# Optimization experiments

Hardware: AMD Instinct MI355X
Metric: run time of the kernel (lower is better)

## Reference

```python
import jax, jax.numpy as jnp
import numpy as np

EPS = 1.0 / 137.0
NUM_HEADS = 16


def yat_dense(x, kernel, bias, alpha):
    y = jnp.einsum('btc,cf->btf', x, kernel)
    x2 = jnp.sum(x * x, axis=-1, keepdims=True)          # [B,T,1]
    k2 = jnp.sum(kernel * kernel, axis=0)                 # [F]
    y = (y * y) / (x2 + k2 - 2.0 * y + EPS)
    out_f = kernel.shape[1]
    scale = (jnp.sqrt(jnp.float32(out_f)) / jnp.log1p(jnp.float32(out_f))) ** alpha
    return y * scale + bias


def setup_inputs() -> dict:
    key = jax.random.key(0)
    ks = jax.random.split(key, 6)
    B, T, C = 2, 1024, 1024
    x = jax.random.normal(ks[0], (B, T, C), dtype=jnp.float32)
    mask = jnp.tril(jnp.ones((T, T), dtype=bool))[None, None, :, :]  # causal [1,1,T,T]
    w_qkv = jax.random.normal(ks[1], (C, 3 * C), dtype=jnp.float32) * 0.02
    b_qkv = jnp.zeros((3 * C,), dtype=jnp.float32)
    alpha_qkv = jnp.ones((1,), dtype=jnp.float32)
    w_proj = jax.random.normal(ks[2], (C, C), dtype=jnp.float32) * 0.02
    b_proj = jnp.zeros((C,), dtype=jnp.float32)
    alpha_proj = jnp.ones((1,), dtype=jnp.float32)
    alpha_attn = jnp.ones((1,), dtype=jnp.float32)
    return {"x": x, "mask": mask, "w_qkv": w_qkv, "b_qkv": b_qkv,
            "alpha_qkv": alpha_qkv, "w_proj": w_proj, "b_proj": b_proj,
            "alpha_proj": alpha_proj, "alpha_attn": alpha_attn}


def reference(x, mask, w_qkv, b_qkv, alpha_qkv, w_proj, b_proj, alpha_proj, alpha_attn):
    B, T, C = x.shape
    head_dim = C // NUM_HEADS
    scale = jnp.log1p(jnp.float32(head_dim))
    inv_scale = (head_dim / scale) ** alpha_attn  # [1]

    qkv = yat_dense(x, w_qkv, b_qkv, alpha_qkv)               # [B,T,3C]
    qkv = qkv.reshape(B, T, 3, NUM_HEADS, head_dim)
    q, k, v = jnp.moveaxis(qkv, 2, 0)                         # each [B,T,H,hd]
    # NOTE: source transposes with (0,3,1,2) -> [B, head_dim, T, H]; reproduced faithfully.
    q = jnp.transpose(q, (0, 3, 1, 2))
    k = jnp.transpose(k, (0, 3, 1, 2))
    v = jnp.transpose(v, (0, 3, 1, 2))

    dot = jnp.einsum('bhid,bhjd->bhij', q, k)                 # [B,hd,T,T]
    sq_dot = dot * dot
    q2 = jnp.sum(q * q, axis=-1, keepdims=True)               # [B,hd,T,1]
    k2 = jnp.sum(k * k, axis=-1, keepdims=True).transpose(0, 1, 3, 2)  # [B,hd,1,T]
    sq_dist = q2 + k2 - 2.0 * dot
    attn = sq_dot / (sq_dist + EPS)
    attn = attn * inv_scale
    attn = jnp.where(mask, attn, jnp.finfo(jnp.float32).min)
    attn = jax.nn.softmax(attn, axis=-1)

    out = jnp.einsum('bhij,bhjd->bhid', attn, v)              # [B,hd,T,H]
    out = out.transpose(0, 2, 1, 3).reshape(B, T, C)
    out = yat_dense(out, w_proj, b_proj, alpha_proj)
    return out
```

## Files before the change

kernel.cpp:

```cpp
#include <hip/hip_runtime.h>
#include <math.h>

#define YAT_EPS (1.0f / 137.0f)


typedef __bf16 bf16x8 __attribute__((ext_vector_type(8)));
typedef float floatx4 __attribute__((ext_vector_type(4)));
typedef unsigned int uintx4 __attribute__((ext_vector_type(4)));

__device__ __forceinline__ float fast_rcp(float x) {
#if __has_builtin(__builtin_amdgcn_rcpf)
    return __builtin_amdgcn_rcpf(x);
#else
    return 1.0f / x;
#endif
}
__device__ __forceinline__ float fast_exp2(float x) {
#if __has_builtin(__builtin_amdgcn_exp2f)
    return __builtin_amdgcn_exp2f(x);
#else
    return exp2f(x);
#endif
}

__device__ __forceinline__ unsigned short f32_bf16(float f) {
    unsigned u = __builtin_bit_cast(unsigned, f);
    u += 0x7fffu + ((u >> 16) & 1u);
    return (unsigned short)(u >> 16);
}
__device__ __forceinline__ float bf16_f32(unsigned short h) {
    unsigned u = ((unsigned)h) << 16;
    return __builtin_bit_cast(float, u);
}

__global__ void convtrans_kernel(
    const float* __restrict__ W, unsigned short* __restrict__ th,
    unsigned short* __restrict__ tl, float* __restrict__ k2, int K, int N)
{
    __shared__ float t[32][33];
    int tx = threadIdx.x, ty = threadIdx.y;
    int n0 = blockIdx.x * 32, k0 = blockIdx.y * 32;
    #pragma unroll
    for (int r = 0; r < 4; ++r)
        t[ty + r * 8][tx] = W[(size_t)(k0 + ty + r * 8) * N + n0 + tx];
    __syncthreads();
    #pragma unroll
    for (int r = 0; r < 4; ++r) {
        int nl = ty + r * 8;
        float v = t[tx][nl];
        unsigned short h = f32_bf16(v);
        th[(size_t)(n0 + nl) * K + k0 + tx] = h;
        tl[(size_t)(n0 + nl) * K + k0 + tx] = f32_bf16(v - bf16_f32(h));
        float s = v * v;
        #pragma unroll
        for (int m = 16; m > 0; m >>= 1) s += __shfl_xor(s, m, 32);
        if (tx == 0) atomicAdd(&k2[n0 + nl], s);
    }
}

__global__ __launch_bounds__(256) void convx_kernel(
    const float* __restrict__ x, unsigned short* __restrict__ hi,
    unsigned short* __restrict__ lo, float* __restrict__ x2x)
{
    __shared__ float red[4];
    const int row = blockIdx.x, tid = threadIdx.x;
    float4 v = *(const float4*)(x + (size_t)row * 1024 + tid * 4);
    float vv[4] = {v.x, v.y, v.z, v.w};
    unsigned short hh[4], ll[4];
    float s = 0.0f;
    #pragma unroll
    for (int e = 0; e < 4; ++e) {
        hh[e] = f32_bf16(vv[e]);
        ll[e] = f32_bf16(vv[e] - bf16_f32(hh[e]));
        s = fmaf(vv[e], vv[e], s);
    }
    *(ushort4*)(hi + (size_t)row * 1024 + tid * 4) =
        make_ushort4(hh[0], hh[1], hh[2], hh[3]);
    *(ushort4*)(lo + (size_t)row * 1024 + tid * 4) =
        make_ushort4(ll[0], ll[1], ll[2], ll[3]);
    #pragma unroll
    for (int off = 32; off > 0; off >>= 1) s += __shfl_down(s, off, 64);
    if ((tid & 63) == 0) red[tid >> 6] = s;
    __syncthreads();
    if (tid == 0) x2x[row] = red[0] + red[1] + red[2] + red[3];
}

template <int BM, int MODE>
__global__ __launch_bounds__(256) void gemm_yat_mfma_kernel(
    const unsigned short* __restrict__ Ah, const unsigned short* __restrict__ Al,
    const unsigned short* __restrict__ Bh, const unsigned short* __restrict__ Bl,
    const float* __restrict__ bias, const float* __restrict__ x2,
    const float* __restrict__ k2, const float* __restrict__ alphap,
    float* __restrict__ out, int N, int K, float scale_base)
{
    constexpr int TM = BM / 32;
    constexpr int NI = (BM * 128 + 16384) / 4096;
    __shared__ __align__(16) unsigned short sbuf[BM * 64 + 8192];

    const int tid = threadIdx.x;
    const int w = tid >> 6, l = tid & 63;
    const int lane16 = l & 15, quad = l >> 4;
    const int wm = w & 1, wn = w >> 1;
    const int m0 = blockIdx.y * BM, n0 = blockIdx.x * 128;

    floatx4 acc[TM][4];
    #pragma unroll
    for (int tm = 0; tm < TM; ++tm)
        #pragma unroll
        for (int tn = 0; tn < 4; ++tn)
            acc[tm][tn] = (floatx4){0.f, 0.f, 0.f, 0.f};

    for (int k0 = 0; k0 < K; k0 += 32) {
        __syncthreads();
        #pragma unroll
        for (int i = 0; i < NI; ++i) {
            const int o = (i * 4 + w) * 1024;
            const unsigned short* gp;
            if (o < BM * 128) {
                const unsigned short* g = (o < BM * 64) ? Ah : Al;
                const int oo = (o < BM * 64) ? o : o - BM * 64;
                gp = g + (size_t)(m0 + (oo >> 6) + (l >> 2)) * K + k0 + (l & 3) * 8;
            } else {
                const int ob = o - BM * 128;
                const unsigned short* g = (ob < 8192) ? Bh : Bl;
                const int oo = ob & 8191;
                gp = g + (size_t)(n0 + (oo >> 6) + (l >> 2)) * K + k0 + (l & 3) * 8;
            }
            __builtin_amdgcn_global_load_lds(
                (const __attribute__((address_space(1))) unsigned int*)gp,
                (__attribute__((address_space(3))) unsigned int*)((char*)sbuf + o),
                16, 0, 0);
        }
        __syncthreads();

        bf16x8 afh[TM], afl[TM], bfh[4], bfl[4];
        #pragma unroll
        for (int tm = 0; tm < TM; ++tm) {
            const int base = (wm * (BM / 2) + tm * 16 + lane16) * 32 + quad * 8;
            afh[tm] = *(const bf16x8*)(sbuf + base);
            afl[tm] = *(const bf16x8*)(sbuf + BM * 32 + base);
        }
        #pragma unroll
        for (int tn = 0; tn < 4; ++tn) {
            const int nb = (wn * 64 + tn * 16 + lane16) * 32 + quad * 8;
            bfh[tn] = *(const bf16x8*)(sbuf + BM * 64 + nb);
            bfl[tn] = *(const bf16x8*)(sbuf + BM * 64 + 4096 + nb);
        }
        #pragma unroll
        for (int tm = 0; tm < TM; ++tm)
            #pragma unroll
            for (int tn = 0; tn < 4; ++tn) {
                acc[tm][tn] = __builtin_amdgcn_mfma_f32_16x16x32_bf16(
                    afh[tm], bfh[tn], acc[tm][tn], 0, 0, 0);
                acc[tm][tn] = __builtin_amdgcn_mfma_f32_16x16x32_bf16(
                    afh[tm], bfl[tn], acc[tm][tn], 0, 0, 0);
                acc[tm][tn] = __builtin_amdgcn_mfma_f32_16x16x32_bf16(
                    afl[tm], bfh[tn], acc[tm][tn], 0, 0, 0);
            }
    }

    const float scale = powf(scale_base, alphap[0]);
    #pragma unroll
    for (int tm = 0; tm < TM; ++tm) {
        #pragma unroll
        for (int tn = 0; tn < 4; ++tn) {
            const int n = n0 + wn * 64 + tn * 16 + lane16;
            const float kk = k2[n];
            const float bb = bias[n];
            const int mrow = m0 + wm * (BM / 2) + tm * 16 + quad * 4;
            float4 r4;
            float* rp = (float*)&r4;
            #pragma unroll
            for (int r = 0; r < 4; ++r) {
                const float y = acc[tm][tn][r];
                const float den = x2[mrow + r] + kk - 2.0f * y + YAT_EPS;
                rp[r] = y * y / den * scale + bb;
            }
            if (MODE == 0) {
                #pragma unroll
                for (int r = 0; r < 4; ++r)
                    out[(size_t)(mrow + r) * N + n] = rp[r];
            } else {
                const int s = n >> 10, hh = (n >> 6) & 15, dd = n & 63;
                const int bb2 = m0 >> 10;
                const int t0 = (mrow & 1023);
                *(float4*)&out[((size_t)((bb2 * 3 + s) * 64 + dd) * 16 + hh)
                               * 1024 + t0] = r4;
            }
        }
    }
}

__global__ __launch_bounds__(256) void prep_q_kernel(
    const float* __restrict__ qkvT, unsigned short* __restrict__ QP,
    float* __restrict__ q2k)
{
    const int idx = blockIdx.x * 256 + threadIdx.x;
    const int b = idx >> 16, dt = idx & 65535;
    const int d = dt >> 10, t = dt & 1023;
    const float* src = qkvT + ((size_t)(b * 3 * 64) + d) * 16384 + t;
    float q[16]; float s2 = 0.f;
    unsigned short hi[16], lo[16];
    #pragma unroll
    for (int h = 0; h < 16; ++h) {
        q[h] = src[h * 1024];
        s2 = fmaf(q[h], q[h], s2);
        hi[h] = f32_bf16(q[h]);
        lo[h] = f32_bf16(q[h] - bf16_f32(hi[h]));
    }
    q2k[idx] = s2;
    unsigned short* dst = QP + (size_t)idx * 32;
    #pragma unroll
    for (int h4 = 0; h4 < 4; ++h4) {
        *(ushort4*)(dst + h4 * 4) =
            make_ushort4(hi[h4*4], hi[h4*4+1], hi[h4*4+2], hi[h4*4+3]);
        *(ushort4*)(dst + 16 + h4 * 4) =
            make_ushort4(lo[h4*4], lo[h4*4+1], lo[h4*4+2], lo[h4*4+3]);
    }
}

__global__ __launch_bounds__(256) void prep_k_kernel(
    const float* __restrict__ qkvT, unsigned short* __restrict__ KP,
    float* __restrict__ k2k)
{
    const int idx = blockIdx.x * 256 + threadIdx.x;
    const int b = idx >> 16, dt = idx & 65535;
    const int d = dt >> 10, t = dt & 1023;
    const float* src = qkvT + ((size_t)((b * 3 + 1) * 64) + d) * 16384 + t;
    float k[16]; float s2 = 0.f;
    unsigned short hi[16], lo[16];
    #pragma unroll
    for (int h = 0; h < 16; ++h) {
        k[h] = src[h * 1024];
        s2 = fmaf(k[h], k[h], s2);
        hi[h] = f32_bf16(k[h]);
        lo[h] = f32_bf16(k[h] - bf16_f32(hi[h]));
    }
    k2k[idx] = s2;
    unsigned short* dst = KP + (size_t)b * 6291456 + (size_t)dt * 32;
    #pragma unroll
    for (int h4 = 0; h4 < 4; ++h4) {
        *(ushort4*)(dst + h4 * 4) =
            make_ushort4(hi[h4*4], hi[h4*4+1], hi[h4*4+2], hi[h4*4+3]);
        *(ushort4*)(dst + 16 + h4 * 4) =
            make_ushort4(lo[h4*4], lo[h4*4+1], lo[h4*4+2], lo[h4*4+3]);
    }
}

__global__ __launch_bounds__(256) void prep_v_kernel(
    const float* __restrict__ qkvT, unsigned short* __restrict__ VP)
{
    const int idx = blockIdx.x * 256 + threadIdx.x;
    const int h = idx & 15;
    const int quad = (idx >> 4) & 3;
    const int jt2 = (idx >> 6) & 31;
    const int d = (idx >> 11) & 63;
    const int b = idx >> 17;
    const float* src = qkvT + ((size_t)((b * 3 + 2) * 64) + d) * 16384
                            + h * 1024 + jt2 * 32 + quad * 4;
    float4 v0 = *(const float4*)(src);
    float4 v1 = *(const float4*)(src + 16);
    float vv[8] = {v0.x, v0.y, v0.z, v0.w, v1.x, v1.y, v1.z, v1.w};
    unsigned short hi[8], lo[8];
    #pragma unroll
    for (int e = 0; e < 8; ++e) {
        hi[e] = f32_bf16(vv[e]);
        lo[e] = f32_bf16(vv[e] - bf16_f32(hi[e]));
    }
    unsigned short* dst = VP + (size_t)b * 6291456 + 2097152
                             + d * 32768 + jt2 * 1024 + quad * 128 + h * 8;
    *(ushort4*)(dst)       = make_ushort4(hi[0], hi[1], hi[2], hi[3]);
    *(ushort4*)(dst + 4)   = make_ushort4(hi[4], hi[5], hi[6], hi[7]);
    *(ushort4*)(dst + 512) = make_ushort4(lo[0], lo[1], lo[2], lo[3]);
    *(ushort4*)(dst + 516) = make_ushort4(lo[4], lo[5], lo[6], lo[7]);
}

__global__ __launch_bounds__(256) void yat_attn_mfma2_kernel(
    const unsigned short* __restrict__ QP,
    const unsigned short* __restrict__ KVU,
    const float* __restrict__ k2k, const float* __restrict__ q2k,
    const float* __restrict__ alphap,
    unsigned short* __restrict__ attn_h, unsigned short* __restrict__ attn_l,
    float* __restrict__ x2a)
{
    const int tid = threadIdx.x;
    const int lane = tid & 63, w = tid >> 6;
    const int lane16 = lane & 15, quad = lane >> 4;
    const int d = blockIdx.x, c = blockIdx.y, b = blockIdx.z;

    const float isc =
        powf(64.0f / log1pf(64.0f), alphap[0]) * 1.44269504f;

    const unsigned short* kp = KVU + (size_t)b * 6291456 + d * 32768;
    const unsigned short* vp = KVU + (size_t)b * 6291456 + 2097152 + d * 32768;
    const unsigned short* qp = QP + (size_t)(b * 65536 + d * 1024) * 32;
    const float* k2bd = k2k + b * 65536 + d * 1024;
    const float* q2bd = q2k + b * 65536 + d * 1024;

    const int ti0 = c * 4 + w;
    const int tiA = ti0, tiB = 63 - ti0;

    const bf16x8 qA = *(const bf16x8*)(qp + (tiA * 16 + lane16) * 32 + quad * 8);
    const bf16x8 qB = *(const bf16x8*)(qp + (tiB * 16 + lane16) * 32 + quad * 8);
    const float q2A = q2bd[tiA * 16 + lane16] + YAT_EPS;
    const float q2B = q2bd[tiB * 16 + lane16] + YAT_EPS;
    const int iA = tiA * 16 + lane16;
    const int iB = tiB * 16 + lane16;

    floatx4 OA = (floatx4){0.f, 0.f, 0.f, 0.f};
    floatx4 OB = (floatx4){0.f, 0.f, 0.f, 0.f};
    float lsA = 0.f, lsB = 0.f;

    const int lastA = tiA >> 1, lastB = tiB >> 1;

    for (int jt2 = 0; jt2 <= lastB; ++jt2) {
        const int j0 = jt2 * 32;
        const unsigned short* kp0 = kp + (j0 + lane16) * 32;
        const unsigned short* kp1 = kp + (j0 + 16 + lane16) * 32;
        const bf16x8 k0a = *(const bf16x8*)(kp0 + quad * 8);
        const bf16x8 k0b = *(const bf16x8*)(kp0 + ((quad ^ 2) * 8));
        const bf16x8 k1a = *(const bf16x8*)(kp1 + quad * 8);
        const bf16x8 k1b = *(const bf16x8*)(kp1 + ((quad ^ 2) * 8));
        const unsigned short* vpj = vp + jt2 * 1024 + quad * 128 + lane16 * 8;
        const bf16x8 vh = *(const bf16x8*)(vpj);
        const bf16x8 vl = *(const bf16x8*)(vpj + 512);
        const float4 k20 = *(const float4*)(k2bd + j0 + quad * 4);
        const float4 k21 = *(const float4*)(k2bd + j0 + 16 + quad * 4);
        const float k2r[8] = {k20.x, k20.y, k20.z, k20.w,
                              k21.x, k21.y, k21.z, k21.w};
        const int jbase0 = j0 + quad * 4;

        #pragma unroll
        for (int half = 0; half < 2; ++half) {
            if (half == 0 && jt2 > lastA) continue;
            const bf16x8 qf = half ? qB : qA;
            const float q2e = half ? q2B : q2A;
            const int iM = half ? iB : iA;
            floatx4 S0 = __builtin_amdgcn_mfma_f32_16x16x32_bf16(
                k0a, qf, (floatx4){0.f, 0.f, 0.f, 0.f}, 0, 0, 0);
            S0 = __builtin_amdgcn_mfma_f32_16x16x32_bf16(k0b, qf, S0, 0, 0, 0);
            floatx4 S1 = __builtin_amdgcn_mfma_f32_16x16x32_bf16(
                k1a, qf, (floatx4){0.f, 0.f, 0.f, 0.f}, 0, 0, 0);
            S1 = __builtin_amdgcn_mfma_f32_16x16x32_bf16(k1b, qf, S1, 0, 0, 0);

            float p[8], lsum = 0.f;
            #pragma unroll
            for (int e = 0; e < 8; ++e) {
                const float s = (e < 4) ? S0[e & 3] : S1[e & 3];
                const int j = jbase0 + (e >> 2) * 16 + (e & 3);
                const float den = fmaf(-2.f, s, q2e + k2r[e]);
                float pe = fast_exp2(s * s * fast_rcp(den) * isc);
                pe = (j <= iM) ? pe : 0.f;
                lsum += pe;
                p[e] = pe;
            }
            if (half) lsB += lsum; else lsA += lsum;

            unsigned ph32[4], pl32[4];
            #pragma unroll
            for (int e2 = 0; e2 < 4; ++e2) {
                const unsigned b0 = __builtin_bit_cast(unsigned, p[e2 * 2]);
                const unsigned b1 = __builtin_bit_cast(unsigned, p[e2 * 2 + 1]);
                const unsigned r0 = b0 + 0x7fffu + ((b0 >> 16) & 1u);
                const unsigned r1 = b1 + 0x7fffu + ((b1 >> 16) & 1u);
                ph32[e2] = (r0 >> 16) | (r1 & 0xFFFF0000u);
                const float f0 = p[e2 * 2] -
                    __builtin_bit_cast(float, r0 & 0xFFFF0000u);
                const float f1 = p[e2 * 2 + 1] -
                    __builtin_bit_cast(float, r1 & 0xFFFF0000u);
                pl32[e2] = (__builtin_bit_cast(unsigned, f0) >> 16) |
                           (__builtin_bit_cast(unsigned, f1) & 0xFFFF0000u);
            }
            const bf16x8 Ph = __builtin_bit_cast(bf16x8,
                (uintx4){ph32[0], ph32[1], ph32[2], ph32[3]});
            const bf16x8 Pl = __builtin_bit_cast(bf16x8,
                (uintx4){pl32[0], pl32[1], pl32[2], pl32[3]});

            floatx4 O = half ? OB : OA;
            O = __builtin_amdgcn_mfma_f32_16x16x32_bf16(Ph, vh, O, 0, 0, 0);
            O = __builtin_amdgcn_mfma_f32_16x16x32_bf16(Pl, vh, O, 0, 0, 0);
            O = __builtin_amdgcn_mfma_f32_16x16x32_bf16(Ph, vl, O, 0, 0, 0);
            if (half) OB = O; else OA = O;
        }
    }

    #pragma unroll
    for (int half = 0; half < 2; ++half) {
        float ls = half ? lsB : lsA;
        const floatx4 O = half ? OB : OA;
        const int ti = half ? tiB : tiA;
        ls += __shfl_xor(ls, 16, 64);
        ls += __shfl_xor(ls, 32, 64);
        const float linv = 1.0f / ls;
        #pragma unroll
        for (int r = 0; r < 4; ++r) {
            const float lr = __shfl(linv, quad * 4 + r, 16);
            const float v = O[r] * lr;
            const int i = ti * 16 + quad * 4 + r;
            const size_t off =
                ((size_t)(b * 1024 + i)) * 1024 + d * 16 + lane16;
            const unsigned short vh16 = f32_bf16(v);
            attn_h[off] = vh16;
            attn_l[off] = f32_bf16(v - bf16_f32(vh16));
            float s2 = v * v;
            s2 += __shfl_xor(s2, 1, 64);
            s2 += __shfl_xor(s2, 2, 64);
            s2 += __shfl_xor(s2, 4, 64);
            s2 += __shfl_xor(s2, 8, 64);
            if (lane16 == 0) atomicAdd(&x2a[b * 1024 + i], s2);
        }
    }
}

extern "C" void kernel_launch(void* const* d_in, const int* in_sizes, int n_in,
                              void* d_out, int out_size, void* d_ws, size_t ws_size,
                              hipStream_t stream)
{
    const float* x          = (const float*)d_in[0];
    const float* w_qkv      = (const float*)d_in[2];
    const float* b_qkv      = (const float*)d_in[3];
    const float* alpha_qkv  = (const float*)d_in[4];
    const float* w_proj     = (const float*)d_in[5];
    const float* b_proj     = (const float*)d_in[6];
    const float* alpha_proj = (const float*)d_in[7];
    const float* alpha_attn = (const float*)d_in[8];
    float* out = (float*)d_out;

    float* ws = (float*)d_ws;
    float*          qkvT = ws;
    unsigned short* WtQh = (unsigned short*)(ws + 6291456);
    unsigned short* WtQl = (unsigned short*)(ws + 7864320);
    unsigned short* WtPh = (unsigned short*)(ws + 9437184);
    unsigned short* WtPl = (unsigned short*)(ws + 9961472);
    unsigned short* xh   = (unsigned short*)(ws + 10485760);
    unsigned short* xl   = (unsigned short*)(ws + 11534336);
    float* x2x  = ws + 12582912;
    float* x2a  = ws + 12584960;
    float* k2q  = ws + 12587008;
    float* k2p  = ws + 12590080;
    float* k2k  = ws + 12591104;
    float* q2k  = ws + 12722176;
    unsigned short* attn_h = WtQh;
    unsigned short* attn_l = WtQl;
    unsigned short* QP = xh;
    unsigned short* KVU = (unsigned short*)qkvT;

    hipMemsetAsync(x2a, 0, (2048 + 3072 + 1024) * sizeof(float), stream);

    convtrans_kernel<<<dim3(96, 32), dim3(32, 8), 0, stream>>>(
        w_qkv, WtQh, WtQl, k2q, 1024, 3072);
    convtrans_kernel<<<dim3(32, 32), dim3(32, 8), 0, stream>>>(
        w_proj, WtPh, WtPl, k2p, 1024, 1024);
    convx_kernel<<<2048, 256, 0, stream>>>(x, xh, xl, x2x);

    const float sb_qkv = sqrtf(3072.0f) / log1pf(3072.0f);
    gemm_yat_mfma_kernel<64, 1><<<dim3(24, 32), 256, 0, stream>>>(
        xh, xl, WtQh, WtQl, b_qkv, x2x, k2q, alpha_qkv, qkvT,
        3072, 1024, sb_qkv);

    prep_q_kernel<<<512, 256, 0, stream>>>(qkvT, QP, q2k);
    prep_k_kernel<<<512, 256, 0, stream>>>(qkvT, KVU, k2k);
    prep_v_kernel<<<1024, 256, 0, stream>>>(qkvT, KVU);

    yat_attn_mfma2_kernel<<<dim3(64, 8, 2), 256, 0, stream>>>(
        QP, KVU, k2k, q2k, alpha_attn, attn_h, attn_l, x2a);

    const float sb_proj = sqrtf(1024.0f) / log1pf(1024.0f);
    gemm_yat_mfma_kernel<64, 0><<<dim3(8, 32), 256, 0, stream>>>(
        attn_h, attn_l, WtPh, WtPl, b_proj, x2a, k2p, alpha_proj, out,
        1024, 1024, sb_proj);
}
```

Baseline: 268.4 us.

## Fuse Q/K/V bf16 packing into QKV GEMM epilogue via permuted weight columns

Permutes the columns of the transposed QKV weight so each 128-wide GEMM tile holds all 16 heads for 8 head dims. The GEMM epilogue stages results through LDS and writes the split-bf16 Q/K/V layouts and squared norms directly. This removes the fp32 qkvT intermediate and the three prep kernels, along with their global memory round trip. The cost is an epilogue with extra syncs, scattered 2-byte stores for V, and Q now sharing the KVU buffer region.

```diff
diff --git a/kernel.cpp b/kernel.cpp
--- a/kernel.cpp
+++ b/kernel.cpp
@@ -33,6 +33,7 @@
     return __builtin_bit_cast(float, u);
 }
 
+template <bool PERM>
 __global__ void convtrans_kernel(
     const float* __restrict__ W, unsigned short* __restrict__ th,
     unsigned short* __restrict__ tl, float* __restrict__ k2, int K, int N)
@@ -47,14 +48,20 @@
     #pragma unroll
     for (int r = 0; r < 4; ++r) {
         int nl = ty + r * 8;
+        int nn = n0 + nl;
+        int nw = nn;
+        if (PERM) {
+            nw = (nn & ~1023) | (((nn & 63) >> 3) << 7)
+               | (((nn >> 6) & 15) << 3) | (nn & 7);
+        }
         float v = t[tx][nl];
         unsigned short h = f32_bf16(v);
-        th[(size_t)(n0 + nl) * K + k0 + tx] = h;
-        tl[(size_t)(n0 + nl) * K + k0 + tx] = f32_bf16(v - bf16_f32(h));
+        th[(size_t)nw * K + k0 + tx] = h;
+        tl[(size_t)nw * K + k0 + tx] = f32_bf16(v - bf16_f32(h));
         float s = v * v;
         #pragma unroll
         for (int m = 16; m > 0; m >>= 1) s += __shfl_xor(s, m, 32);
-        if (tx == 0) atomicAdd(&k2[n0 + nl], s);
+        if (tx == 0) atomicAdd(&k2[nn], s);
     }
 }
 
@@ -91,7 +98,9 @@
     const unsigned short* __restrict__ Bh, const unsigned short* __restrict__ Bl,
     const float* __restrict__ bias, const float* __restrict__ x2,
     const float* __restrict__ k2, const float* __restrict__ alphap,
-    float* __restrict__ out, int N, int K, float scale_base)
+    float* __restrict__ out, int N, int K, float scale_base,
+    unsigned short* __restrict__ kvu, float* __restrict__ q2k,
+    float* __restrict__ k2k)
 {
     constexpr int TM = BM / 32;
     constexpr int NI = (BM * 128 + 16384) / 4096;
@@ -160,123 +169,110 @@
     }
 
     const float scale = powf(scale_base, alphap[0]);
-    #pragma unroll
-    for (int tm = 0; tm < TM; ++tm) {
-        #pragma unroll
-        for (int tn = 0; tn < 4; ++tn) {
-            const int n = n0 + wn * 64 + tn * 16 + lane16;
-            const float kk = k2[n];
-            const float bb = bias[n];
-            const int mrow = m0 + wm * (BM / 2) + tm * 16 + quad * 4;
-            float4 r4;
-            float* rp = (float*)&r4;
+
+    if (MODE == 0) {
+        #pragma unroll
+        for (int tm = 0; tm < TM; ++tm) {
             #pragma unroll
-            for (int r = 0; r < 4; ++r) {
-                const float y = acc[tm][tn][r];
-                const float den = x2[mrow + r] + kk - 2.0f * y + YAT_EPS;
-                rp[r] = y * y / den * scale + bb;
-            }
-            if (MODE == 0) {
+            for (int tn = 0; tn < 4; ++tn) {
+                const int n = n0 + wn * 64 + tn * 16 + lane16;
+                const float kk = k2[n];
+                const float bb = bias[n];
+                const int mrow = m0 + wm * (BM / 2) + tm * 16 + quad * 4;
                 #pragma unroll
-                for (int r = 0; r < 4; ++r)
-                    out[(size_t)(mrow + r) * N + n] = rp[r];
+                for (int r = 0; r < 4; ++r) {
+                    const float y = acc[tm][tn][r];
+                    const float den = x2[mrow + r] + kk - 2.0f * y + YAT_EPS;
+                    out[(size_t)(mrow + r) * N + n] =
+                        y * y / den * scale + bb;
+                }
+            }
+        }
+    } else {
+        float* lds = (float*)sbuf;
+        const int s_ = n0 >> 10;
+        const int dblk = (n0 >> 7) & 7;
+        const int b_ = m0 >> 10;
+        const int tl = tid >> 3;
+        const int ddr = tid & 7;
+        const int d_glob = dblk * 8 + ddr;
+
+        #pragma unroll
+        for (int half = 0; half < 2; ++half) {
+            __syncthreads();
+            if (wm == half) {
+                #pragma unroll
+                for (int tm = 0; tm < TM; ++tm) {
+                    #pragma unroll
+                    for (int tn = 0; tn < 4; ++tn) {
+                        const int n = n0 + wn * 64 + tn * 16 + lane16;
+                        const int hcol = (n >> 3) & 15;
+                        const int norig = (n & ~1023) | (hcol << 6)
+                                        | (dblk << 3) | (n & 7);
+                        const float kk = k2[norig];
+                        const float bb = bias[norig];
+                        const int mrow = m0 + wm * 32 + tm * 16 + quad * 4;
+                        const int tbase = tm * 16 + quad * 4;
+                        const int col = wn * 64 + tn * 16 + lane16;
+                        #pragma unroll
+                        for (int r = 0; r < 4; ++r) {
+                            const float y = acc[tm][tn][r];
+                            const float den =
+                                x2[mrow + r] + kk - 2.0f * y + YAT_EPS;
+                            lds[(tbase + r) * 132 + col] =
+                                y * y / den * scale + bb;
+                        }
+                    }
+                }
+            }
+            __syncthreads();
+
+            float y[16];
+            #pragma unroll
+            for (int h = 0; h < 16; ++h)
+                y[h] = lds[tl * 132 + h * 8 + ddr];
+            const int t_glob = (m0 & 1023) + half * 32 + tl;
+
+            if (s_ < 2) {
+                unsigned short hb[16], lb[16];
+                float s2 = 0.f;
+                #pragma unroll
+                for (int h = 0; h < 16; ++h) {
+                    hb[h] = f32_bf16(y[h]);
+                    lb[h] = f32_bf16(y[h] - bf16_f32(hb[h]));
+                    s2 = fmaf(y[h], y[h], s2);
+                }
+                unsigned short* dst = kvu + (size_t)b_ * 6291456
+                    + (s_ == 0 ? 4194304u : 0u)
+                    + ((size_t)(d_glob * 1024 + t_glob)) * 32;
+                #pragma unroll
+                for (int h4 = 0; h4 < 4; ++h4) {
+                    *(ushort4*)(dst + h4 * 4) = make_ushort4(
+                        hb[h4*4], hb[h4*4+1], hb[h4*4+2], hb[h4*4+3]);
+                    *(ushort4*)(dst + 16 + h4 * 4) = make_ushort4(
+                        lb[h4*4], lb[h4*4+1], lb[h4*4+2], lb[h4*4+3]);
+                }
+                float* sq = (s_ == 0) ? q2k : k2k;
+                sq[b_ * 65536 + d_glob * 1024 + t_glob] = s2;
             } else {
-                const int s = n >> 10, hh = (n >> 6) & 15, dd = n & 63;
-                const int bb2 = m0 >> 10;
-                const int t0 = (mrow & 1023);
-                *(float4*)&out[((size_t)((bb2 * 3 + s) * 64 + dd) * 16 + hh)
-                               * 1024 + t0] = r4;
-            }
-        }
-    }
-}
-
-__global__ __launch_bounds__(256) void prep_q_kernel(
-    const float* __restrict__ qkvT, unsigned short* __restrict__ QP,
-    float* __restrict__ q2k)
-{
-    const int idx = blockIdx.x * 256 + threadIdx.x;
-    const int b = idx >> 16, dt = idx & 65535;
-    const int d = dt >> 10, t = dt & 1023;
-    const float* src = qkvT + ((size_t)(b * 3 * 64) + d) * 16384 + t;
-    float q[16]; float s2 = 0.f;
-    unsigned short hi[16], lo[16];
-    #pragma unroll
-    for (int h = 0; h < 16; ++h) {
-        q[h] = src[h * 1024];
-        s2 = fmaf(q[h], q[h], s2);
-        hi[h] = f32_bf16(q[h]);
-        lo[h] = f32_bf16(q[h] - bf16_f32(hi[h]));
-    }
-    q2k[idx] = s2;
-    unsigned short* dst = QP + (size_t)idx * 32;
-    #pragma unroll
-    for (int h4 = 0; h4 < 4; ++h4) {
-        *(ushort4*)(dst + h4 * 4) =
-            make_ushort4(hi[h4*4], hi[h4*4+1], hi[h4*4+2], hi[h4*4+3]);
-        *(ushort4*)(dst + 16 + h4 * 4) =
-            make_ushort4(lo[h4*4], lo[h4*4+1], lo[h4*4+2], lo[h4*4+3]);
-    }
-}
-
-__global__ __launch_bounds__(256) void prep_k_kernel(
-    const float* __restrict__ qkvT, unsigned short* __restrict__ KP,
-    float* __restrict__ k2k)
-{
-    const int idx = blockIdx.x * 256 + threadIdx.x;
-    const int b = idx >> 16, dt = idx & 65535;
-    const int d = dt >> 10, t = dt & 1023;
-    const float* src = qkvT + ((size_t)((b * 3 + 1) * 64) + d) * 16384 + t;
-    float k[16]; float s2 = 0.f;
-    unsigned short hi[16], lo[16];
-    #pragma unroll
-    for (int h = 0; h < 16; ++h) {
-        k[h] = src[h * 1024];
-        s2 = fmaf(k[h], k[h], s2);
-        hi[h] = f32_bf16(k[h]);
-        lo[h] = f32_bf16(k[h] - bf16_f32(hi[h]));
-    }
-    k2k[idx] = s2;
-    unsigned short* dst = KP + (size_t)b * 6291456 + (size_t)dt * 32;
-    #pragma unroll
-    for (int h4 = 0; h4 < 4; ++h4) {
-        *(ushort4*)(dst + h4 * 4) =
-            make_ushort4(hi[h4*4], hi[h4*4+1], hi[h4*4+2], hi[h4*4+3]);
-        *(ushort4*)(dst + 16 + h4 * 4) =
-            make_ushort4(lo[h4*4], lo[h4*4+1], lo[h4*4+2], lo[h4*4+3]);
-    }
-}
-
-__global__ __launch_bounds__(256) void prep_v_kernel(
-    const float* __restrict__ qkvT, unsigned short* __restrict__ VP)
-{
-    const int idx = blockIdx.x * 256 + threadIdx.x;
-    const int h = idx & 15;
-    const int quad = (idx >> 4) & 3;
-    const int jt2 = (idx >> 6) & 31;
-    const int d = (idx >> 11) & 63;
-    const int b = idx >> 17;
-    const float* src = qkvT + ((size_t)((b * 3 + 2) * 64) + d) * 16384
-                            + h * 1024 + jt2 * 32 + quad * 4;
-    float4 v0 = *(const float4*)(src);
-    float4 v1 = *(const float4*)(src + 16);
-    float vv[8] = {v0.x, v0.y, v0.z, v0.w, v1.x, v1.y, v1.z, v1.w};
-    unsigned short hi[8], lo[8];
-    #pragma unroll
-    for (int e = 0; e < 8; ++e) {
-        hi[e] = f32_bf16(vv[e]);
-        lo[e] = f32_bf16(vv[e] - bf16_f32(hi[e]));
-    }
-    unsigned short* dst = VP + (size_t)b * 6291456 + 2097152
-                             + d * 32768 + jt2 * 1024 + quad * 128 + h * 8;
-    *(ushort4*)(dst)       = make_ushort4(hi[0], hi[1], hi[2], hi[3]);
-    *(ushort4*)(dst + 4)   = make_ushort4(hi[4], hi[5], hi[6], hi[7]);
-    *(ushort4*)(dst + 512) = make_ushort4(lo[0], lo[1], lo[2], lo[3]);
-    *(ushort4*)(dst + 516) = make_ushort4(lo[4], lo[5], lo[6], lo[7]);
+                const int j = t_glob;
+                const int jt2 = j >> 5;
+                const int e = ((j >> 4) & 1) * 4 + (j & 3);
+                const int qd = (j >> 2) & 3;
+                unsigned short* dst = kvu + (size_t)b_ * 6291456 + 2097152
+                    + d_glob * 32768 + jt2 * 1024 + qd * 128 + e;
+                #pragma unroll
+                for (int h = 0; h < 16; ++h) {
+                    const unsigned short vh = f32_bf16(y[h]);
+                    dst[h * 8] = vh;
+                    dst[512 + h * 8] = f32_bf16(y[h] - bf16_f32(vh));
+                }
+            }
+        }
+    }
 }
 
 __global__ __launch_bounds__(256) void yat_attn_mfma2_kernel(
-    const unsigned short* __restrict__ QP,
     const unsigned short* __restrict__ KVU,
     const float* __restrict__ k2k, const float* __restrict__ q2k,
     const float* __restrict__ alphap,
@@ -293,7 +289,7 @@
 
     const unsigned short* kp = KVU + (size_t)b * 6291456 + d * 32768;
     const unsigned short* vp = KVU + (size_t)b * 6291456 + 2097152 + d * 32768;
-    const unsigned short* qp = QP + (size_t)(b * 65536 + d * 1024) * 32;
+    const unsigned short* qp = KVU + (size_t)b * 6291456 + 4194304 + d * 32768;
     const float* k2bd = k2k + b * 65536 + d * 1024;
     const float* q2bd = q2k + b * 65536 + d * 1024;
 
@@ -427,7 +423,7 @@
     float* out = (float*)d_out;
 
     float* ws = (float*)d_ws;
-    float*          qkvT = ws;
+    unsigned short* KVU  = (unsigned short*)ws;
     unsigned short* WtQh = (unsigned short*)(ws + 6291456);
     unsigned short* WtQl = (unsigned short*)(ws + 7864320);
     unsigned short* WtPh = (unsigned short*)(ws + 9437184);
@@ -442,31 +438,25 @@
     float* q2k  = ws + 12722176;
     unsigned short* attn_h = WtQh;
     unsigned short* attn_l = WtQl;
-    unsigned short* QP = xh;
-    unsigned short* KVU = (unsigned short*)qkvT;
 
     hipMemsetAsync(x2a, 0, (2048 + 3072 + 1024) * sizeof(float), stream);
 
-    convtrans_kernel<<<dim3(96, 32), dim3(32, 8), 0, stream>>>(
+    convtrans_kernel<true><<<dim3(96, 32), dim3(32, 8), 0, stream>>>(
         w_qkv, WtQh, WtQl, k2q, 1024, 3072);
-    convtrans_kernel<<<dim3(32, 32), dim3(32, 8), 0, stream>>>(
+    convtrans_kernel<false><<<dim3(32, 32), dim3(32, 8), 0, stream>>>(
         w_proj, WtPh, WtPl, k2p, 1024, 1024);
     convx_kernel<<<2048, 256, 0, stream>>>(x, xh, xl, x2x);
 
     const float sb_qkv = sqrtf(3072.0f) / log1pf(3072.0f);
-    gemm_yat_mfma_kernel<64, 1><<<dim3(24, 32), 256, 0, stream>>>(
-        xh, xl, WtQh, WtQl, b_qkv, x2x, k2q, alpha_qkv, qkvT,
-        3072, 1024, sb_qkv);
-
-    prep_q_kernel<<<512, 256, 0, stream>>>(qkvT, QP, q2k);
-    prep_k_kernel<<<512, 256, 0, stream>>>(qkvT, KVU, k2k);
-    prep_v_kernel<<<1024, 256, 0, stream>>>(qkvT, KVU);
+    gemm_yat_mfma_kernel<64, 2><<<dim3(24, 32), 256, 0, stream>>>(
+        xh, xl, WtQh, WtQl, b_qkv, x2x, k2q, alpha_qkv, nullptr,
+        3072, 1024, sb_qkv, KVU, q2k, k2k);
 
     yat_attn_mfma2_kernel<<<dim3(64, 8, 2), 256, 0, stream>>>(
-        QP, KVU, k2k, q2k, alpha_attn, attn_h, attn_l, x2a);
+        KVU, k2k, q2k, alpha_attn, attn_h, attn_l, x2a);
 
     const float sb_proj = sqrtf(1024.0f) / log1pf(1024.0f);
     gemm_yat_mfma_kernel<64, 0><<<dim3(8, 32), 256, 0, stream>>>(
         attn_h, attn_l, WtPh, WtPl, b_proj, x2a, k2p, alpha_proj, out,
-        1024, 1024, sb_proj);
-}
+        1024, 1024, sb_proj, nullptr, nullptr, nullptr);
+}
```

New measurement: 252.2 us. 6.0% less time.
